# Performance work log

Hardware: AMD Instinct MI355X
Metric: run time of the kernel (lower is better)

## Reference

```python
import jax, jax.numpy as jnp
import numpy as np

B, S, D, H = 4, 2048, 1024, 16
HD = D // H
DFF = 4 * D
EPS = 1e-5


def gelu_tanh(x):
    c = jnp.sqrt(jnp.asarray(2.0 / jnp.pi, x.dtype))
    return 0.5 * x * (1.0 + jnp.tanh(c * (x + 0.044715 * x ** 3)))


def layernorm(x, scale, shift):
    mean = jnp.mean(x, axis=-1, keepdims=True)
    var = jnp.var(x, axis=-1, keepdims=True)  # unbiased=False
    return scale * (x - mean) * jax.lax.rsqrt(var + EPS) + shift


def setup_inputs() -> dict:
    key = jax.random.key(0)
    ks = jax.random.split(key, 12)
    s_in = 1.0 / np.sqrt(D)
    s_ff = 1.0 / np.sqrt(DFF)
    return {
        "x": jax.random.normal(ks[0], (B, S, D), jnp.float32),
        "Wq": jax.random.uniform(ks[1], (D, D), jnp.float32, -s_in, s_in),
        "Wk": jax.random.uniform(ks[2], (D, D), jnp.float32, -s_in, s_in),
        "Wv": jax.random.uniform(ks[3], (D, D), jnp.float32, -s_in, s_in),
        "Wo": jax.random.uniform(ks[4], (D, D), jnp.float32, -s_in, s_in),
        "bo": jax.random.uniform(ks[5], (D,), jnp.float32, -s_in, s_in),
        "W1": jax.random.uniform(ks[6], (D, DFF), jnp.float32, -s_in, s_in),
        "b1": jax.random.uniform(ks[7], (DFF,), jnp.float32, -s_in, s_in),
        "W2": jax.random.uniform(ks[8], (DFF, D), jnp.float32, -s_ff, s_ff),
        "b2": jax.random.uniform(ks[9], (D,), jnp.float32, -s_ff, s_ff),
        "ln1_scale": jnp.ones((D,), jnp.float32),
        "ln1_shift": jnp.zeros((D,), jnp.float32),
        "ln2_scale": jnp.ones((D,), jnp.float32),
        "ln2_shift": jnp.zeros((D,), jnp.float32),
    }


def reference(x, Wq, Wk, Wv, Wo, bo, W1, b1, W2, b2,
              ln1_scale, ln1_shift, ln2_scale, ln2_shift):
    # --- pre-LN causal MHA ---
    h = layernorm(x, ln1_scale, ln1_shift)
    q = (h @ Wq).reshape(B, S, H, HD).transpose(0, 2, 1, 3)  # [B,H,S,hd]
    k = (h @ Wk).reshape(B, S, H, HD).transpose(0, 2, 1, 3)
    v = (h @ Wv).reshape(B, S, H, HD).transpose(0, 2, 1, 3)
    scores = jnp.einsum('bhqd,bhkd->bhqk', q, k)
    causal = jnp.tril(jnp.ones((S, S), bool))  # mask strict upper triangle
    scores = jnp.where(causal, scores, -jnp.inf)
    attn = jax.nn.softmax(scores / np.sqrt(HD), axis=-1)
    ctx = jnp.einsum('bhqk,bhkd->bhqd', attn, v)
    ctx = ctx.transpose(0, 2, 1, 3).reshape(B, S, D)
    x = x + (ctx @ Wo + bo)
    # --- FFN ---
    h = layernorm(x, ln2_scale, ln2_shift)
    h = gelu_tanh(h @ W1 + b1) @ W2 + b2
    return x + h
```

## Files before the change

### kernel.cpp

```cpp
#include <hip/hip_runtime.h>
#include <math.h>

#define S_LEN  2048
#define DMODEL 1024
#define NHEAD  16
#define BATCH  4
#define NROWS  (BATCH*S_LEN)
#define DFF    4096
#define QKV_LD 3072

typedef __attribute__((ext_vector_type(4))) unsigned short us4;
typedef __attribute__((ext_vector_type(8))) unsigned short us8;
typedef __attribute__((ext_vector_type(8))) __bf16 bf16x8;
typedef __attribute__((ext_vector_type(4))) float f32x4;

#if __has_builtin(__builtin_amdgcn_exp2f)
#define EXP2(x) __builtin_amdgcn_exp2f(x)
#else
#define EXP2(x) exp2f(x)
#endif
#if __has_builtin(__builtin_amdgcn_rcpf)
#define RCP(x) __builtin_amdgcn_rcpf(x)
#else
#define RCP(x) (1.0f/(x))
#endif

static __device__ __forceinline__ unsigned short f2bf(float f) {
  __bf16 b = (__bf16)f;
  return __builtin_bit_cast(unsigned short, b);
}
#define GLD16(gp, lp) __builtin_amdgcn_global_load_lds( \
    (const __attribute__((address_space(1))) unsigned int*)(gp), \
    (__attribute__((address_space(3))) unsigned int*)(lp), 16, 0, 0)

static __device__ __forceinline__ int xcd_swz(int bid, int nwg) {
  int q = nwg >> 3;
  return (bid & 7) * q + (bid >> 3);
}

__global__ __launch_bounds__(256) void ln_kernel(
    const float* __restrict__ x, const float* __restrict__ scale,
    const float* __restrict__ shift, unsigned short* __restrict__ out)
{
  const int row = blockIdx.x, tid = threadIdx.x;
  const int lane = tid & 63, wave = tid >> 6;
  const float* xr = x + (size_t)row * DMODEL;
  f32x4 v = *(const f32x4*)&xr[tid * 4];
  float s  = v[0]+v[1]+v[2]+v[3];
  float s2 = v[0]*v[0]+v[1]*v[1]+v[2]*v[2]+v[3]*v[3];
  #pragma unroll
  for (int m = 1; m < 64; m <<= 1) { s += __shfl_xor(s, m); s2 += __shfl_xor(s2, m); }
  __shared__ float red[8];
  if (lane == 0) { red[wave] = s; red[4 + wave] = s2; }
  __syncthreads();
  s  = red[0]+red[1]+red[2]+red[3];
  s2 = red[4]+red[5]+red[6]+red[7];
  float mean = s * (1.0f/DMODEL);
  float var  = s2 * (1.0f/DMODEL) - mean*mean;
  float rstd = rsqrtf(var + 1e-5f);
  us4 o;
  #pragma unroll
  for (int j = 0; j < 4; j++) {
    float val = (v[j]-mean)*rstd*scale[tid*4+j] + shift[tid*4+j];
    o[j] = f2bf(val);
  }
  *(us4*)&out[(size_t)row*DMODEL + tid*4] = o;
}

__global__ __launch_bounds__(256) void wtrans_all(
    const float* __restrict__ Wq, const float* __restrict__ Wk,
    const float* __restrict__ Wv, const float* __restrict__ Wo,
    const float* __restrict__ W1, const float* __restrict__ W2,
    unsigned short* __restrict__ wqkvt, unsigned short* __restrict__ wot,
    unsigned short* __restrict__ w1t, unsigned short* __restrict__ w2t,
    float sclq)
{
  __shared__ unsigned short tile[64][72];
  const int bid = blockIdx.x, tid = threadIdx.x;
  const float* W; unsigned short* Wt; int K, N, sub; float scl = 1.0f;
  if (bid < 1024) {
    int wsel = bid >> 8; sub = bid & 255; K = 1024; N = 1024;
    W  = (wsel == 0) ? Wq : (wsel == 1) ? Wk : (wsel == 2) ? Wv : Wo;
    Wt = (wsel == 0) ? wqkvt : (wsel == 1) ? wqkvt + 1024*1024
       : (wsel == 2) ? wqkvt + 2048*1024 : wot;
    if (wsel == 0) scl = sclq;
  } else if (bid < 2048) { sub = bid - 1024; K = 1024; N = 4096; W = W1; Wt = w1t; }
  else                   { sub = bid - 2048; K = 4096; N = 1024; W = W2; Wt = w2t; }
  const int nbn = N >> 6;
  const int kt = sub / nbn, nt = sub % nbn;
  int r = tid >> 2, c0 = (tid & 3) << 4;
  const float* src = W + (size_t)(kt*64 + r)*N + nt*64 + c0;
  #pragma unroll
  for (int j = 0; j < 16; j += 4) {
    f32x4 f = *(const f32x4*)&src[j];
    tile[r][c0+j+0] = f2bf(f[0]*scl); tile[r][c0+j+1] = f2bf(f[1]*scl);
    tile[r][c0+j+2] = f2bf(f[2]*scl); tile[r][c0+j+3] = f2bf(f[3]*scl);
  }
  __syncthreads();
  int n = tid >> 2, k0 = (tid & 3) << 4;
  us8 o0, o1;
  #pragma unroll
  for (int j = 0; j < 8; j++) { o0[j] = tile[k0+j][n]; o1[j] = tile[k0+8+j][n]; }
  unsigned short* dst = Wt + (size_t)(nt*64 + n)*K + kt*64 + k0;
  *(us8*)&dst[0] = o0;
  *(us8*)&dst[8] = o1;
}

__global__ __launch_bounds__(256) void vtrans(
    const unsigned short* __restrict__ v, unsigned short* __restrict__ vt)
{
  __shared__ unsigned short tile[64][72];
  const int tid = threadIdx.x;
  const int bh = blockIdx.x >> 5, st = blockIdx.x & 31;
  const int b = bh >> 4, h = bh & 15;
  int r = tid >> 2, c0 = (tid & 3) << 4;
  const unsigned short* src = v + (size_t)(b*S_LEN + st*64 + r)*QKV_LD + h*64 + c0;
  *(us8*)&tile[r][c0]   = *(const us8*)&src[0];
  *(us8*)&tile[r][c0+8] = *(const us8*)&src[8];
  __syncthreads();
  int d = tid >> 2, s0 = (tid & 3) << 4;
  us8 o0, o1;
  #pragma unroll
  for (int j = 0; j < 8; j++) { o0[j] = tile[s0+j][d]; o1[j] = tile[s0+8+j][d]; }
  unsigned short* dst = vt + (size_t)(bh*64 + d)*S_LEN + st*64 + s0;
  *(us8*)&dst[0] = o0;
  *(us8*)&dst[8] = o1;
}

template<bool BIAS, bool RESID, bool GELU_, bool OUTF32>
__global__ __launch_bounds__(256, 3) void gemm_bt(
    const unsigned short* __restrict__ A, const unsigned short* __restrict__ Bt,
    void* Cout, const float* __restrict__ bias, const float* resid,
    int M, int N, int K)
{
  __shared__ unsigned short sA[128*64];
  __shared__ unsigned short sB[128*64];
  const int tid = threadIdx.x;
  const int wave = tid >> 6, lane = tid & 63;
  const int l15 = lane & 15, g = lane >> 4, x7 = lane & 7;
  const int nbn = N >> 7;
  const int bid = xcd_swz(blockIdx.x, gridDim.x);
  const int bm = bid / nbn, bn = bid % nbn;
  const int wr = (wave >> 1) << 6, wc = (wave & 1) << 6;

  f32x4 acc[4][4] = {};

  const int rrow = lane >> 3;
  const int srcc = (x7 ^ rrow) << 3;
  const unsigned short* ga0 = A  + (size_t)(bm*128 + rrow)*K + srcc;
  const unsigned short* gb0 = Bt + (size_t)(bn*128 + rrow)*K + srcc;

  for (int kb = 0; kb < K; kb += 64) {
    #pragma unroll
    for (int i = 0; i < 4; i++) {
      int rr = (wave*4 + i) * 8;
      GLD16(ga0 + (size_t)rr*K + kb, &sA[rr*64]);
      GLD16(gb0 + (size_t)rr*K + kb, &sB[rr*64]);
    }
    __syncthreads();
    #pragma unroll
    for (int kk = 0; kk < 2; kk++) {
      const int csw = ((kk*4 + g) ^ x7) << 3;
      bf16x8 af[4], bfr[4];
      #pragma unroll
      for (int m = 0; m < 4; m++)
        af[m] = *(const bf16x8*)&sA[(wr + m*16 + l15)*64 + csw];
      #pragma unroll
      for (int n = 0; n < 4; n++)
        bfr[n] = *(const bf16x8*)&sB[(wc + n*16 + l15)*64 + csw];
      #pragma unroll
      for (int m = 0; m < 4; m++)
        #pragma unroll
        for (int n = 0; n < 4; n++)
          acc[m][n] = __builtin_amdgcn_mfma_f32_16x16x32_bf16(af[m], bfr[n], acc[m][n], 0, 0, 0);
    }
    __syncthreads();
  }

  #pragma unroll
  for (int m = 0; m < 4; m++) {
    #pragma unroll
    for (int r = 0; r < 4; r++) {
      int grow = bm*128 + wr + m*16 + g*4 + r;
      #pragma unroll
      for (int n = 0; n < 4; n++) {
        int gcol = bn*128 + wc + n*16 + l15;
        float v = acc[m][n][r];
        if (BIAS) v += bias[gcol];
        if (GELU_) {
          float xx = v;
          float u = 0.7978845608f*(xx + 0.044715f*xx*xx*xx);
          float e = EXP2(u * 2.88539008f);
          float th = 1.0f - 2.0f*RCP(e + 1.0f);
          v = 0.5f*xx*(1.0f + th);
        }
        if (RESID) v += resid[(size_t)grow*N + gcol];
        if (OUTF32) ((float*)Cout)[(size_t)grow*N + gcol] = v;
        else ((unsigned short*)Cout)[(size_t)grow*N + gcol] = f2bf(v);
      }
    }
  }
}

template<bool BIAS, bool GELU_>
__global__ __launch_bounds__(512, 2) void gemm256(
    const unsigned short* __restrict__ A, const unsigned short* __restrict__ Bt,
    unsigned short* __restrict__ Cout, const float* __restrict__ bias,
    int M, int N, int K)
{
  constexpr int BN = 256, WN = 64, NF = 4;
  __shared__ unsigned short sA[2][256*64];
  __shared__ unsigned short sB[2][BN*64];
  const int tid = threadIdx.x;
  const int wave = tid >> 6, lane = tid & 63;
  const int wm = wave >> 2, wn = wave & 3;
  const int l15 = lane & 15, g = lane >> 4, x7 = lane & 7, r8 = lane >> 3;
  const int srcc = (x7 ^ r8) << 3;
  const int nbn = N / BN;
  const int bid = xcd_swz(blockIdx.x, gridDim.x);
  const int bm = bid / nbn, bn = bid % nbn;
  const unsigned short* gA = A  + (size_t)(bm*256)*K;
  const unsigned short* gB = Bt + (size_t)(bn*BN)*K;
  const int NT = K >> 6;

  f32x4 acc[8][NF] = {};

#define STAGEA(buf, h, kb) do { \
    _Pragma("unroll") \
    for (int j_ = 0; j_ < 2; j_++) \
      GLD16(gA + (size_t)((h)*128 + j_*64 + wave*8 + r8)*K + (kb) + srcc, \
            &sA[buf][((h)*128 + j_*64 + wave*8)*64]); \
  } while (0)
#define STAGEB(buf, h, kb) do { \
    _Pragma("unroll") \
    for (int j_ = 0; j_ < 2; j_++) \
      GLD16(gB + (size_t)((h)*128 + j_*64 + wave*8 + r8)*K + (kb) + srcc, \
            &sB[buf][((h)*128 + j_*64 + wave*8)*64]); \
  } while (0)
#define RDA_(m, kk) (*(const bf16x8*)&cA[(wm*128 + (m)*16 + l15)*64 + ((((kk)*4+g)^x7)<<3)])
#define RDB_(n, kk) (*(const bf16x8*)&cB[(wn*WN + (n)*16 + l15)*64 + ((((kk)*4+g)^x7)<<3)])
#define PH(p) do { \
    __builtin_amdgcn_s_setprio(1); \
    _Pragma("unroll") for (int mm_ = 0; mm_ < 2; mm_++) \
    _Pragma("unroll") for (int n_ = 0; n_ < NF; n_++) \
    _Pragma("unroll") for (int kk_ = 0; kk_ < 2; kk_++) \
      acc[(p)*2+mm_][n_] = __builtin_amdgcn_mfma_f32_16x16x32_bf16( \
          af[mm_][kk_], bfr[n_][kk_], acc[(p)*2+mm_][n_], 0, 0, 0); \
    __builtin_amdgcn_s_setprio(0); \
  } while (0)

  STAGEB(0, 0, 0); STAGEB(0, 1, 0);
  STAGEA(0, 0, 0); STAGEA(0, 1, 0);
  STAGEB(1, 0, 64); STAGEB(1, 1, 64);

  for (int t = 0; t < NT; ++t) {
    const int c = t & 1;
    const unsigned short* cA = sA[c];
    const unsigned short* cB = sB[c];
    const int kb1 = (t + 1) * 64, kb2 = (t + 2) * 64;
    bf16x8 af[2][2], bfr[NF][2];

    if (t < NT - 1) asm volatile("s_waitcnt vmcnt(4)" ::: "memory");
    else            asm volatile("s_waitcnt vmcnt(0)" ::: "memory");
    __builtin_amdgcn_s_barrier();
    __builtin_amdgcn_sched_barrier(0);

    #pragma unroll
    for (int n = 0; n < NF; n++) { bfr[n][0] = RDB_(n, 0); bfr[n][1] = RDB_(n, 1); }
    af[0][0] = RDA_(0, 0); af[0][1] = RDA_(0, 1);
    af[1][0] = RDA_(1, 0); af[1][1] = RDA_(1, 1);
    if (t + 1 < NT) STAGEA(c ^ 1, 0, kb1);
    PH(0);
    af[0][0] = RDA_(2, 0); af[0][1] = RDA_(2, 1);
    af[1][0] = RDA_(3, 0); af[1][1] = RDA_(3, 1);
    if (t + 1 < NT) STAGEA(c ^ 1, 1, kb1);
    PH(1);
    __builtin_amdgcn_s_barrier();
    af[0][0] = RDA_(4, 0); af[0][1] = RDA_(4, 1);
    af[1][0] = RDA_(5, 0); af[1][1] = RDA_(5, 1);
    if (t + 2 < NT) STAGEB(c, 0, kb2);
    PH(2);
    af[0][0] = RDA_(6, 0); af[0][1] = RDA_(6, 1);
    af[1][0] = RDA_(7, 0); af[1][1] = RDA_(7, 1);
    if (t + 2 < NT) STAGEB(c, 1, kb2);
    PH(3);
  }

  #pragma unroll
  for (int m = 0; m < 8; m++) {
    #pragma unroll
    for (int r = 0; r < 4; r++) {
      int grow = bm*256 + wm*128 + m*16 + g*4 + r;
      #pragma unroll
      for (int n = 0; n < NF; n++) {
        int gcol = bn*BN + wn*WN + n*16 + l15;
        float v = acc[m][n][r];
        if (BIAS) v += bias[gcol];
        if (GELU_) {
          float xx = v;
          float u = 0.7978845608f*(xx + 0.044715f*xx*xx*xx);
          float e = EXP2(u * 2.88539008f);
          float th = 1.0f - 2.0f*RCP(e + 1.0f);
          v = 0.5f*xx*(1.0f + th);
        }
        Cout[(size_t)grow*N + gcol] = f2bf(v);
      }
    }
  }
#undef STAGEA
#undef STAGEB
#undef RDA_
#undef RDB_
#undef PH
}

__global__ __launch_bounds__(512) void attn_kernel(
    const unsigned short* __restrict__ qb, const unsigned short* __restrict__ kb,
    const unsigned short* __restrict__ vt, unsigned short* __restrict__ ctx)
{
  __shared__ unsigned short sK[2][64*64];
  __shared__ unsigned short sV[2][64*64];
  __shared__ unsigned short sP[8][16*64];
  const int tid = threadIdx.x, wave = tid >> 6, lane = tid & 63;
  const int l15 = lane & 15, g = lane >> 4, x7 = lane & 7;
  const int qt = 15 - (blockIdx.x >> 6);
  const int bh = blockIdx.x & 63;
  const int b = bh >> 4, h = bh & 15;
  const int qrow = qt*128 + wave*16;
  const int NTI = 2*qt + 2;

  bf16x8 qf[2];
  {
    const unsigned short* qr = qb + (size_t)(b*S_LEN + qrow + l15) * QKV_LD + h*64;
    qf[0] = *(const bf16x8*)&qr[g*8];
    qf[1] = *(const bf16x8*)&qr[32 + g*8];
  }

  us8 ones_u;
  #pragma unroll
  for (int j = 0; j < 8; j++) ones_u[j] = 0x3F80;
  const bf16x8 ones8 = __builtin_bit_cast(bf16x8, ones_u);

  f32x4 oacc[4] = {};
  f32x4 lacc = {};
  float mrow[4];
  #pragma unroll
  for (int r = 0; r < 4; r++) mrow[r] = -INFINITY;

  const int rrow = lane >> 3;
  const int srcc = (x7 ^ rrow) << 3;
  const unsigned short* kbase = kb + (size_t)(b*S_LEN)*QKV_LD + h*64 + srcc;
  const unsigned short* vbase = vt + (size_t)(bh*64)*S_LEN + srcc;

#define ASTAGE(buf, t) do { \
    const int kv0_ = (t)*64; \
    GLD16(kbase + (size_t)(kv0_ + wave*8 + rrow)*QKV_LD, &sK[buf][wave*8*64]); \
    GLD16(vbase + (size_t)(wave*8 + rrow)*S_LEN + kv0_,  &sV[buf][wave*8*64]); \
  } while(0)

  ASTAGE(0, 0);

  for (int t = 0; t < NTI; ++t) {
    __syncthreads();
    const int cur = t & 1;
    if (t < NTI - 1) ASTAGE(cur ^ 1, t + 1);

    const int kv0 = t*64;
    if (kv0 > qrow + 15) continue;

    f32x4 sacc[4] = {};
    __builtin_amdgcn_s_setprio(1);
    #pragma unroll
    for (int kk = 0; kk < 2; kk++) {
      const int csw = ((kk*4 + g) ^ x7) << 3;
      #pragma unroll
      for (int n = 0; n < 4; n++) {
        bf16x8 kf = *(const bf16x8*)&sK[cur][(n*16 + l15)*64 + csw];
        sacc[n] = __builtin_amdgcn_mfma_f32_16x16x32_bf16(qf[kk], kf, sacc[n], 0, 0, 0);
      }
    }
    __builtin_amdgcn_s_setprio(0);

    float p[4][4], rm[4];
    const bool masked = (kv0 + 63 > qrow);
    #pragma unroll
    for (int r = 0; r < 4; r++) {
      float m_ = -INFINITY;
      #pragma unroll
      for (int n = 0; n < 4; n++) {
        float sc = sacc[n][r];
        if (masked && (kv0 + n*16 + l15) > (qrow + g*4 + r)) sc = -INFINITY;
        p[n][r] = sc;
        m_ = fmaxf(m_, sc);
      }
      rm[r] = m_;
    }
    bool need = (rm[0] > mrow[0] + 8.0f) | (rm[1] > mrow[1] + 8.0f) |
                (rm[2] > mrow[2] + 8.0f) | (rm[3] > mrow[3] + 8.0f);
    if (__any(need)) {
      #pragma unroll
      for (int r = 0; r < 4; r++) {
        float vv = rm[r];
        vv = fmaxf(vv, __shfl_xor(vv, 1));
        vv = fmaxf(vv, __shfl_xor(vv, 2));
        vv = fmaxf(vv, __shfl_xor(vv, 4));
        vv = fmaxf(vv, __shfl_xor(vv, 8));
        float mn = fmaxf(mrow[r], vv);
        float alpha = EXP2(mrow[r] - mn);
        mrow[r] = mn;
        lacc[r] *= alpha;
        #pragma unroll
        for (int nd = 0; nd < 4; nd++) oacc[nd][r] *= alpha;
      }
    }
    #pragma unroll
    for (int n = 0; n < 4; n++)
      #pragma unroll
      for (int r = 0; r < 4; r++)
        p[n][r] = EXP2(p[n][r] - mrow[r]);

    #pragma unroll
    for (int n = 0; n < 4; n++) {
      const int chunk = n*2 + (l15 >> 3);
      #pragma unroll
      for (int r = 0; r < 4; r++) {
        const int prow = g*4 + r;
        sP[wave][prow*64 + ((chunk ^ (prow & 7)) << 3) + x7] = f2bf(p[n][r]);
      }
    }
    asm volatile("s_waitcnt lgkmcnt(0)" ::: "memory");
    __builtin_amdgcn_sched_barrier(0);

    __builtin_amdgcn_s_setprio(1);
    #pragma unroll
    for (int kk = 0; kk < 2; kk++) {
      const int csw = ((kk*4 + g) ^ x7) << 3;
      bf16x8 pa = *(const bf16x8*)&sP[wave][l15*64 + csw];
      #pragma unroll
      for (int nd = 0; nd < 4; nd++) {
        bf16x8 vf = *(const bf16x8*)&sV[cur][(nd*16 + l15)*64 + csw];
        oacc[nd] = __builtin_amdgcn_mfma_f32_16x16x32_bf16(pa, vf, oacc[nd], 0, 0, 0);
      }
      lacc = __builtin_amdgcn_mfma_f32_16x16x32_bf16(pa, ones8, lacc, 0, 0, 0);
    }
    __builtin_amdgcn_s_setprio(0);
  }

  #pragma unroll
  for (int r = 0; r < 4; r++) {
    float inv = RCP(lacc[r]);
    size_t row = (size_t)(b*S_LEN + qrow + g*4 + r);
    #pragma unroll
    for (int nd = 0; nd < 4; nd++)
      ctx[row*DMODEL + h*64 + nd*16 + l15] = f2bf(oacc[nd][r] * inv);
  }
}

extern "C" void kernel_launch(void* const* d_in, const int* in_sizes, int n_in,
                              void* d_out, int out_size, void* d_ws, size_t ws_size,
                              hipStream_t stream)
{
  const float* x    = (const float*)d_in[0];
  const float* Wq   = (const float*)d_in[1];
  const float* Wk   = (const float*)d_in[2];
  const float* Wv   = (const float*)d_in[3];
  const float* Wo   = (const float*)d_in[4];
  const float* bo   = (const float*)d_in[5];
  const float* W1   = (const float*)d_in[6];
  const float* b1   = (const float*)d_in[7];
  const float* W2   = (const float*)d_in[8];
  const float* b2   = (const float*)d_in[9];
  const float* ln1s = (const float*)d_in[10];
  const float* ln1b = (const float*)d_in[11];
  const float* ln2s = (const float*)d_in[12];
  const float* ln2b = (const float*)d_in[13];
  float* out = (float*)d_out;
  (void)in_sizes; (void)n_in; (void)out_size; (void)ws_size;

  char* ws = (char*)d_ws;
  size_t off = 0;
  auto alloc = [&](size_t n) { char* p = ws + off; off += (n + 255) & ~(size_t)255; return p; };
  unsigned short* hbuf  = (unsigned short*)alloc((size_t)NROWS*DMODEL*2);
  unsigned short* qkv   = (unsigned short*)alloc((size_t)NROWS*QKV_LD*2);
  unsigned short* vtb   = (unsigned short*)alloc((size_t)NROWS*DMODEL*2);
  unsigned short* ctx   = (unsigned short*)alloc((size_t)NROWS*DMODEL*2);
  unsigned short* ffn1  = (unsigned short*)alloc((size_t)NROWS*DFF*2);
  unsigned short* wqkvt = (unsigned short*)alloc((size_t)QKV_LD*DMODEL*2);
  unsigned short* wot   = (unsigned short*)alloc((size_t)DMODEL*DMODEL*2);
  unsigned short* w1t   = (unsigned short*)alloc((size_t)DFF*DMODEL*2);
  unsigned short* w2t   = (unsigned short*)alloc((size_t)DMODEL*DFF*2);

  const float SCLQ = 0.18033688011f;

  wtrans_all<<<dim3(3072), dim3(256), 0, stream>>>(
      Wq, Wk, Wv, Wo, W1, W2, wqkvt, wot, w1t, w2t, SCLQ);

  ln_kernel<<<dim3(NROWS), dim3(256), 0, stream>>>(x, ln1s, ln1b, hbuf);
  gemm256<false,false><<<dim3(32*12), dim3(512), 0, stream>>>(
      hbuf, wqkvt, qkv, nullptr, NROWS, QKV_LD, DMODEL);
  vtrans<<<dim3(2048), dim3(256), 0, stream>>>(qkv + 2048, vtb);
  attn_kernel<<<dim3(1024), dim3(512), 0, stream>>>(qkv, qkv + 1024, vtb, ctx);
  gemm_bt<true,true,false,true><<<dim3(64*8), dim3(256), 0, stream>>>(
      ctx, wot, (void*)out, bo, x, NROWS, DMODEL, DMODEL);
  ln_kernel<<<dim3(NROWS), dim3(256), 0, stream>>>(out, ln2s, ln2b, hbuf);
  gemm256<true,true><<<dim3(32*16), dim3(512), 0, stream>>>(
      hbuf, w1t, ffn1, b1, NROWS, DFF, DMODEL);
  gemm_bt<true,true,false,true><<<dim3(64*8), dim3(256), 0, stream>>>(
      ffn1, w2t, (void*)out, b2, out, NROWS, DMODEL, DFF);
}
```

Baseline: 371.0 us.

## Replace single-buffered gemm_bt with double-buffered 128x256 pipelined GEMM for N=1024 projections

The Wo and W2 projections (N=1024) move from a 256-thread, 128x128-tile GEMM with synchronous load/compute to a new 512-thread 128x256-tile kernel. The new kernel double-buffers the A and B tiles in LDS and issues async global-to-LDS loads one or two k-steps ahead, using vmcnt waits and raw barriers. It also splits the MFMA work into two prioritized phases so loads overlap with compute. The grid drops from 512 to 256 blocks, which may underfill a 256-CU device at 2 blocks per CU. Hand-placed waitcnt barriers also carry correctness risk.

```diff
diff --git a/kernel.cpp b/kernel.cpp
--- a/kernel.cpp
+++ b/kernel.cpp
@@ -125,81 +125,6 @@
   unsigned short* dst = vt + (size_t)(bh*64 + d)*S_LEN + st*64 + s0;
   *(us8*)&dst[0] = o0;
   *(us8*)&dst[8] = o1;
-}
-
-template<bool BIAS, bool RESID, bool GELU_, bool OUTF32>
-__global__ __launch_bounds__(256, 3) void gemm_bt(
-    const unsigned short* __restrict__ A, const unsigned short* __restrict__ Bt,
-    void* Cout, const float* __restrict__ bias, const float* resid,
-    int M, int N, int K)
-{
-  __shared__ unsigned short sA[128*64];
-  __shared__ unsigned short sB[128*64];
-  const int tid = threadIdx.x;
-  const int wave = tid >> 6, lane = tid & 63;
-  const int l15 = lane & 15, g = lane >> 4, x7 = lane & 7;
-  const int nbn = N >> 7;
-  const int bid = xcd_swz(blockIdx.x, gridDim.x);
-  const int bm = bid / nbn, bn = bid % nbn;
-  const int wr = (wave >> 1) << 6, wc = (wave & 1) << 6;
-
-  f32x4 acc[4][4] = {};
-
-  const int rrow = lane >> 3;
-  const int srcc = (x7 ^ rrow) << 3;
-  const unsigned short* ga0 = A  + (size_t)(bm*128 + rrow)*K + srcc;
-  const unsigned short* gb0 = Bt + (size_t)(bn*128 + rrow)*K + srcc;
-
-  for (int kb = 0; kb < K; kb += 64) {
-    #pragma unroll
-    for (int i = 0; i < 4; i++) {
-      int rr = (wave*4 + i) * 8;
-      GLD16(ga0 + (size_t)rr*K + kb, &sA[rr*64]);
-      GLD16(gb0 + (size_t)rr*K + kb, &sB[rr*64]);
-    }
-    __syncthreads();
-    #pragma unroll
-    for (int kk = 0; kk < 2; kk++) {
-      const int csw = ((kk*4 + g) ^ x7) << 3;
-      bf16x8 af[4], bfr[4];
-      #pragma unroll
-      for (int m = 0; m < 4; m++)
-        af[m] = *(const bf16x8*)&sA[(wr + m*16 + l15)*64 + csw];
-      #pragma unroll
-      for (int n = 0; n < 4; n++)
-        bfr[n] = *(const bf16x8*)&sB[(wc + n*16 + l15)*64 + csw];
-      #pragma unroll
-      for (int m = 0; m < 4; m++)
-        #pragma unroll
-        for (int n = 0; n < 4; n++)
-          acc[m][n] = __builtin_amdgcn_mfma_f32_16x16x32_bf16(af[m], bfr[n], acc[m][n], 0, 0, 0);
-    }
-    __syncthreads();
-  }
-
-  #pragma unroll
-  for (int m = 0; m < 4; m++) {
-    #pragma unroll
-    for (int r = 0; r < 4; r++) {
-      int grow = bm*128 + wr + m*16 + g*4 + r;
-      #pragma unroll
-      for (int n = 0; n < 4; n++) {
-        int gcol = bn*128 + wc + n*16 + l15;
-        float v = acc[m][n][r];
-        if (BIAS) v += bias[gcol];
-        if (GELU_) {
-          float xx = v;
-          float u = 0.7978845608f*(xx + 0.044715f*xx*xx*xx);
-          float e = EXP2(u * 2.88539008f);
-          float th = 1.0f - 2.0f*RCP(e + 1.0f);
-          v = 0.5f*xx*(1.0f + th);
-        }
-        if (RESID) v += resid[(size_t)grow*N + gcol];
-        if (OUTF32) ((float*)Cout)[(size_t)grow*N + gcol] = v;
-        else ((unsigned short*)Cout)[(size_t)grow*N + gcol] = f2bf(v);
-      }
-    }
-  }
 }
 
 template<bool BIAS, bool GELU_>
@@ -314,6 +239,111 @@
 #undef PH
 }
 
+template<bool BIAS, bool GELU_, bool RESID, bool OUTF32>
+__global__ __launch_bounds__(512, 2) void gemm128(
+    const unsigned short* __restrict__ A, const unsigned short* __restrict__ Bt,
+    void* Cout, const float* __restrict__ bias, const float* resid,
+    int M, int N, int K)
+{
+  __shared__ unsigned short sA[2][128*64];
+  __shared__ unsigned short sB[2][256*64];
+  const int tid = threadIdx.x;
+  const int wave = tid >> 6, lane = tid & 63;
+  const int wm = wave >> 2, wn = wave & 3;
+  const int l15 = lane & 15, g = lane >> 4, x7 = lane & 7, r8 = lane >> 3;
+  const int srcc = (x7 ^ r8) << 3;
+  const int nbn = N >> 8;
+  const int bid = xcd_swz(blockIdx.x, gridDim.x);
+  const int bm = bid / nbn, bn = bid % nbn;
+  const unsigned short* gA = A  + (size_t)(bm*128)*K;
+  const unsigned short* gB = Bt + (size_t)(bn*256)*K;
+  const int NT = K >> 6;
+
+  f32x4 acc[4][4] = {};
+
+#define STAGEA1(buf, kb) do { \
+    _Pragma("unroll") \
+    for (int j_ = 0; j_ < 2; j_++) \
+      GLD16(gA + (size_t)(j_*64 + wave*8 + r8)*K + (kb) + srcc, \
+            &sA[buf][(j_*64 + wave*8)*64]); \
+  } while (0)
+#define STAGEB1(buf, kb) do { \
+    _Pragma("unroll") \
+    for (int j_ = 0; j_ < 4; j_++) \
+      GLD16(gB + (size_t)(j_*64 + wave*8 + r8)*K + (kb) + srcc, \
+            &sB[buf][(j_*64 + wave*8)*64]); \
+  } while (0)
+#define RDA1(m, kk) (*(const bf16x8*)&cA[(wm*64 + (m)*16 + l15)*64 + ((((kk)*4+g)^x7)<<3)])
+#define RDB1(n, kk) (*(const bf16x8*)&cB[(wn*64 + (n)*16 + l15)*64 + ((((kk)*4+g)^x7)<<3)])
+#define PH1(p) do { \
+    __builtin_amdgcn_s_setprio(1); \
+    _Pragma("unroll") for (int mm_ = 0; mm_ < 2; mm_++) \
+    _Pragma("unroll") for (int n_ = 0; n_ < 4; n_++) \
+    _Pragma("unroll") for (int kk_ = 0; kk_ < 2; kk_++) \
+      acc[(p)*2+mm_][n_] = __builtin_amdgcn_mfma_f32_16x16x32_bf16( \
+          af[mm_][kk_], bfr[n_][kk_], acc[(p)*2+mm_][n_], 0, 0, 0); \
+    __builtin_amdgcn_s_setprio(0); \
+  } while (0)
+
+  STAGEB1(0, 0);
+  STAGEA1(0, 0);
+  STAGEB1(1, 64);
+
+  for (int t = 0; t < NT; ++t) {
+    const int c = t & 1;
+    const unsigned short* cA = sA[c];
+    const unsigned short* cB = sB[c];
+    const int kb1 = (t + 1) * 64, kb2 = (t + 2) * 64;
+    bf16x8 af[2][2], bfr[4][2];
+
+    if (t < NT - 1) asm volatile("s_waitcnt vmcnt(4)" ::: "memory");
+    else            asm volatile("s_waitcnt vmcnt(0)" ::: "memory");
+    __builtin_amdgcn_s_barrier();
+    __builtin_amdgcn_sched_barrier(0);
+
+    #pragma unroll
+    for (int n = 0; n < 4; n++) { bfr[n][0] = RDB1(n, 0); bfr[n][1] = RDB1(n, 1); }
+    af[0][0] = RDA1(0, 0); af[0][1] = RDA1(0, 1);
+    af[1][0] = RDA1(1, 0); af[1][1] = RDA1(1, 1);
+    if (t + 1 < NT) STAGEA1(c ^ 1, kb1);
+    PH1(0);
+    __builtin_amdgcn_s_barrier();
+    af[0][0] = RDA1(2, 0); af[0][1] = RDA1(2, 1);
+    af[1][0] = RDA1(3, 0); af[1][1] = RDA1(3, 1);
+    if (t + 2 < NT) STAGEB1(c, kb2);
+    PH1(1);
+  }
+
+  #pragma unroll
+  for (int m = 0; m < 4; m++) {
+    #pragma unroll
+    for (int r = 0; r < 4; r++) {
+      int grow = bm*128 + wm*64 + m*16 + g*4 + r;
+      #pragma unroll
+      for (int n = 0; n < 4; n++) {
+        int gcol = bn*256 + wn*64 + n*16 + l15;
+        float v = acc[m][n][r];
+        if (BIAS) v += bias[gcol];
+        if (GELU_) {
+          float xx = v;
+          float u = 0.7978845608f*(xx + 0.044715f*xx*xx*xx);
+          float e = EXP2(u * 2.88539008f);
+          float th = 1.0f - 2.0f*RCP(e + 1.0f);
+          v = 0.5f*xx*(1.0f + th);
+        }
+        if (RESID) v += resid[(size_t)grow*N + gcol];
+        if (OUTF32) ((float*)Cout)[(size_t)grow*N + gcol] = v;
+        else ((unsigned short*)Cout)[(size_t)grow*N + gcol] = f2bf(v);
+      }
+    }
+  }
+#undef STAGEA1
+#undef STAGEB1
+#undef RDA1
+#undef RDB1
+#undef PH1
+}
+
 __global__ __launch_bounds__(512) void attn_kernel(
     const unsigned short* __restrict__ qb, const unsigned short* __restrict__ kb,
     const unsigned short* __restrict__ vt, unsigned short* __restrict__ ctx)
@@ -500,11 +530,11 @@
       hbuf, wqkvt, qkv, nullptr, NROWS, QKV_LD, DMODEL);
   vtrans<<<dim3(2048), dim3(256), 0, stream>>>(qkv + 2048, vtb);
   attn_kernel<<<dim3(1024), dim3(512), 0, stream>>>(qkv, qkv + 1024, vtb, ctx);
-  gemm_bt<true,true,false,true><<<dim3(64*8), dim3(256), 0, stream>>>(
+  gemm128<true,false,true,true><<<dim3(64*4), dim3(512), 0, stream>>>(
       ctx, wot, (void*)out, bo, x, NROWS, DMODEL, DMODEL);
   ln_kernel<<<dim3(NROWS), dim3(256), 0, stream>>>(out, ln2s, ln2b, hbuf);
   gemm256<true,true><<<dim3(32*16), dim3(512), 0, stream>>>(
       hbuf, w1t, ffn1, b1, NROWS, DFF, DMODEL);
-  gemm_bt<true,true,false,true><<<dim3(64*8), dim3(256), 0, stream>>>(
+  gemm128<true,false,true,true><<<dim3(64*4), dim3(512), 0, stream>>>(
       ffn1, w2t, (void*)out, b2, out, NROWS, DMODEL, DFF);
 }
```

Result: faster. 357.5 us (median of 2 runs) (-3.6%).
